# Optimization experiments

Hardware: AMD Instinct MI355X
Metric: run time of the kernel (lower is better)

## Reference

```python
import jax, jax.numpy as jnp
import numpy as np

D_MODEL = 768
D_STATE = 16
D_CONV = 4
EXPAND = 2
D_INNER = EXPAND * D_MODEL
DT_RANK = (D_MODEL + 15) // 16  # 48
BATCH = 2
SEQ = 1024
LN_EPS = 1e-5


def setup_inputs() -> dict:
    key = jax.random.key(0)
    ks = jax.random.split(key, 12)
    s = 0.02
    inp = {
        "x": jax.random.normal(ks[0], (BATCH, SEQ, D_MODEL), dtype=jnp.float32),
        "in_proj_w": jax.random.normal(ks[1], (2 * D_INNER, D_MODEL), dtype=jnp.float32) * s,
        "conv_w": jax.random.normal(ks[2], (D_INNER, D_CONV), dtype=jnp.float32) * s,
        "conv_b": jnp.zeros((D_INNER,), dtype=jnp.float32),
        "x_proj_w": jax.random.normal(ks[3], (DT_RANK + 2 * D_STATE, D_INNER), dtype=jnp.float32) * s,
        "dt_proj_w": jax.random.normal(ks[4], (D_INNER, DT_RANK), dtype=jnp.float32) * s,
        "dt_proj_b": jnp.full((D_INNER,), -4.0, dtype=jnp.float32),  # softplus(-4) ~ small dt
        "A_log": jnp.log(jnp.broadcast_to(jnp.arange(1, D_STATE + 1, dtype=jnp.float32), (D_INNER, D_STATE))),
        "D": jnp.ones((D_INNER,), dtype=jnp.float32),
        "out_proj_w": jax.random.normal(ks[5], (D_MODEL, D_INNER), dtype=jnp.float32) * s,
        "ln_w": jnp.ones((D_MODEL,), dtype=jnp.float32),
        "ln_b": jnp.zeros((D_MODEL,), dtype=jnp.float32),
    }
    return inp


def _mamba(x, in_proj_w, conv_w, conv_b, x_proj_w, dt_proj_w, dt_proj_b, A_log, D, out_proj_w):
    B, L, _ = x.shape
    # input projection -> [B, L, 2*D_INNER], split into x-branch and gate z
    xz = jnp.einsum("bld,ed->ble", x, in_proj_w)
    xb, z = jnp.split(xz, 2, axis=-1)
    # causal depthwise conv1d along L
    lhs = jnp.transpose(xb, (0, 2, 1))  # [B, D_INNER, L]
    rhs = conv_w[:, None, :]  # [D_INNER, 1, D_CONV]
    xc = jax.lax.conv_general_dilated(
        lhs, rhs, window_strides=(1,), padding=[(D_CONV - 1, 0)],
        dimension_numbers=("NCH", "OIH", "NCH"), feature_group_count=D_INNER)
    xc = jnp.transpose(xc, (0, 2, 1)) + conv_b  # [B, L, D_INNER]
    xc = jax.nn.silu(xc)
    # data-dependent SSM parameters
    x_dbl = jnp.einsum("bld,ed->ble", xc, x_proj_w)  # [B, L, DT_RANK+2*D_STATE]
    dt, Bm, Cm = jnp.split(x_dbl, [DT_RANK, DT_RANK + D_STATE], axis=-1)
    dt = jax.nn.softplus(jnp.einsum("blr,dr->bld", dt, dt_proj_w) + dt_proj_b)  # [B, L, D_INNER]
    A = -jnp.exp(A_log)  # [D_INNER, D_STATE]

    # selective scan over time
    def step(h, inp):
        dt_t, B_t, C_t, u_t = inp  # [B,D_INNER], [B,D_STATE], [B,D_STATE], [B,D_INNER]
        dA = jnp.exp(dt_t[:, :, None] * A)  # [B, D_INNER, D_STATE]
        h = h * dA + (dt_t * u_t)[:, :, None] * B_t[:, None, :]
        y = jnp.einsum("bds,bs->bd", h, C_t)
        return h, y

    h0 = jnp.zeros((B, D_INNER, D_STATE), dtype=x.dtype)
    xs = (jnp.transpose(dt, (1, 0, 2)), jnp.transpose(Bm, (1, 0, 2)),
          jnp.transpose(Cm, (1, 0, 2)), jnp.transpose(xc, (1, 0, 2)))
    _, ys = jax.lax.scan(step, h0, xs)  # ys: [L, B, D_INNER]
    y = jnp.transpose(ys, (1, 0, 2)) + xc * D
    y = y * jax.nn.silu(z)
    return jnp.einsum("ble,de->bld", y, out_proj_w)  # [B, L, D_MODEL]


def reference(x, in_proj_w, conv_w, conv_b, x_proj_w, dt_proj_w, dt_proj_b,
              A_log, D, out_proj_w, ln_w, ln_b):
    residual = x
    h = _mamba(x, in_proj_w, conv_w, conv_b, x_proj_w, dt_proj_w, dt_proj_b, A_log, D, out_proj_w)
    # dropout is identity in eval mode
    y = h + residual
    mu = jnp.mean(y, axis=-1, keepdims=True)
    var = jnp.mean(jnp.square(y - mu), axis=-1, keepdims=True)
    return (y - mu) * jax.lax.rsqrt(var + LN_EPS) * ln_w + ln_b
```

## Files before the change

kernel.cpp:

```cpp
#include <hip/hip_runtime.h>
#include <hip/hip_bf16.h>
#include <math.h>

#define BATCH   2
#define SEQ     1024
#define DMODEL  768
#define DINNER  1536
#define DSTATE  16
#define DTRANK  48
#define NTOK    (BATCH*SEQ)
#define XPROJ_N (DTRANK + 2*DSTATE)

#define LC      64
#define NC      (SEQ/LC)

typedef unsigned short ushort_t;
typedef __attribute__((ext_vector_type(8))) short bf16x8;
typedef __attribute__((ext_vector_type(4))) float f32x4;

__device__ __forceinline__ ushort_t f2bf(float f) {
    unsigned int u = __float_as_uint(f);
    u += 0x7FFF + ((u >> 16) & 1);
    return (ushort_t)(u >> 16);
}

__global__ __launch_bounds__(256)
void f2b_3(const float* __restrict__ s0, ushort_t* __restrict__ d0, int n0,
           const float* __restrict__ s1, ushort_t* __restrict__ d1, int n1,
           const float* __restrict__ s2, ushort_t* __restrict__ d2, int n2)
{
    const int i = (blockIdx.x * 256 + threadIdx.x) * 4;
    const float* s; ushort_t* d;
    if (i < n0)               { s = s0 + i;            d = d0 + i; }
    else if (i < n0 + n1)     { s = s1 + (i - n0);     d = d1 + (i - n0); }
    else if (i < n0 + n1 + n2){ s = s2 + (i - n0 - n1);d = d2 + (i - n0 - n1); }
    else return;
    const float4 v = *reinterpret_cast<const float4*>(s);
    ushort4 o;
    o.x = f2bf(v.x); o.y = f2bf(v.y); o.z = f2bf(v.z); o.w = f2bf(v.w);
    *reinterpret_cast<ushort4*>(d) = o;
}

#define GLOAD_LDS16(gp, lp) \
    __builtin_amdgcn_global_load_lds((const __attribute__((address_space(1))) void*)(gp), \
                                     (__attribute__((address_space(3))) void*)(lp), 16, 0, 0)

__global__ __launch_bounds__(256)
void gemm_mfma_bt(const ushort_t* __restrict__ A, const ushort_t* __restrict__ W,
                  float* __restrict__ C, int M, int N, int K)
{
    __shared__ ushort_t As[128 * 32];
    __shared__ ushort_t Bs[128 * 32];

    const int tid  = threadIdx.x;
    const int w    = tid >> 6;
    const int lane = tid & 63;
    const int m0 = blockIdx.y * 128;
    const int n0 = blockIdx.x * 128;

    const int lrow = lane >> 2;
    const int lcol = (lane & 3) * 8;

    const ushort_t* ga0 = A + (size_t)(m0 + w * 16 + lrow) * K + lcol;
    const ushort_t* ga1 = ga0 + (size_t)64 * K;
    const ushort_t* gb0 = W + (size_t)(n0 + w * 16 + lrow) * K + lcol;
    const ushort_t* gb1 = gb0 + (size_t)64 * K;

    ushort_t* lA0 = As + w * 512;
    ushort_t* lA1 = As + 64 * 32 + w * 512;
    ushort_t* lB0 = Bs + w * 512;
    ushort_t* lB1 = Bs + 64 * 32 + w * 512;

    const int wm = w >> 1, wn = w & 1;
    const int fr = lane & 15;
    const int kg = lane >> 4;

    f32x4 acc[4][4] = {};

    for (int kt = 0; kt < K; kt += 32) {
        __syncthreads();
        GLOAD_LDS16(ga0 + kt, lA0);
        GLOAD_LDS16(ga1 + kt, lA1);
        GLOAD_LDS16(gb0 + kt, lB0);
        GLOAD_LDS16(gb1 + kt, lB1);
        __syncthreads();

        bf16x8 af[4], bfr[4];
        #pragma unroll
        for (int i = 0; i < 4; ++i) {
            af[i]  = *reinterpret_cast<const bf16x8*>(&As[(wm * 64 + i * 16 + fr) * 32 + kg * 8]);
            bfr[i] = *reinterpret_cast<const bf16x8*>(&Bs[(wn * 64 + i * 16 + fr) * 32 + kg * 8]);
        }
        #pragma unroll
        for (int i = 0; i < 4; ++i)
            #pragma unroll
            for (int j = 0; j < 4; ++j)
                acc[i][j] = __builtin_amdgcn_mfma_f32_16x16x32_bf16(af[i], bfr[j], acc[i][j], 0, 0, 0);
    }

    #pragma unroll
    for (int i = 0; i < 4; ++i) {
        const int row_base = m0 + wm * 64 + i * 16 + kg * 4;
        #pragma unroll
        for (int j = 0; j < 4; ++j) {
            const int col = n0 + wn * 64 + j * 16 + fr;
            #pragma unroll
            for (int r = 0; r < 4; ++r)
                C[(size_t)(row_base + r) * N + col] = acc[i][j][r];
        }
    }
}

#define BM 64
#define BN 64
#define BK 16

template<int ACT>
__global__ __launch_bounds__(256)
void gemm_tn(const float* __restrict__ A, const float* __restrict__ W,
             const float* __restrict__ bias, float* __restrict__ C,
             int M, int N, int K, int lda)
{
    __shared__ float As[BK][BM + 4];
    __shared__ float Ws[BK][BN + 4];

    const int t  = threadIdx.x;
    const int tx = t & 15;
    const int ty = t >> 4;
    const int row0 = blockIdx.y * BM;
    const int col0 = blockIdx.x * BN;

    const int m_l = t >> 2;
    const int k_l = (t & 3) * 4;

    float acc[4][4] = {};

    for (int kt = 0; kt < K; kt += BK) {
        float4 av, wv;
        {
            const float* ap = A + (size_t)(row0 + m_l) * lda + kt + k_l;
            av = *reinterpret_cast<const float4*>(ap);
        }
        {
            const int wn = col0 + m_l;
            if (wn < N) {
                const float* wp = W + (size_t)wn * K + kt + k_l;
                wv = *reinterpret_cast<const float4*>(wp);
            } else {
                wv = make_float4(0.f, 0.f, 0.f, 0.f);
            }
        }
        __syncthreads();
        As[k_l + 0][m_l] = av.x; As[k_l + 1][m_l] = av.y;
        As[k_l + 2][m_l] = av.z; As[k_l + 3][m_l] = av.w;
        Ws[k_l + 0][m_l] = wv.x; Ws[k_l + 1][m_l] = wv.y;
        Ws[k_l + 2][m_l] = wv.z; Ws[k_l + 3][m_l] = wv.w;
        __syncthreads();

        #pragma unroll
        for (int k = 0; k < BK; ++k) {
            float4 a4 = *reinterpret_cast<const float4*>(&As[k][ty * 4]);
            float4 w4 = *reinterpret_cast<const float4*>(&Ws[k][tx * 4]);
            float af[4] = {a4.x, a4.y, a4.z, a4.w};
            float wf[4] = {w4.x, w4.y, w4.z, w4.w};
            #pragma unroll
            for (int i = 0; i < 4; ++i)
                #pragma unroll
                for (int j = 0; j < 4; ++j)
                    acc[i][j] += af[i] * wf[j];
        }
    }

    #pragma unroll
    for (int i = 0; i < 4; ++i) {
        const int m = row0 + ty * 4 + i;
        #pragma unroll
        for (int j = 0; j < 4; ++j) {
            const int n = col0 + tx * 4 + j;
            if (n < N) {
                float v = acc[i][j];
                if (ACT == 1) {
                    v += bias[n];
                    v = (v > 20.f) ? v : log1pf(expf(v));
                }
                C[(size_t)m * N + n] = v;
            }
        }
    }
}

__global__ __launch_bounds__(256)
void gemm_tn_splitk(const float* __restrict__ A, const float* __restrict__ W,
                    float* __restrict__ C, int M, int N, int K, int lda, int kchunk)
{
    __shared__ float As[BK][BM + 4];
    __shared__ float Ws[BK][BN + 4];

    const int t  = threadIdx.x;
    const int tx = t & 15;
    const int ty = t >> 4;
    const int row0 = blockIdx.y * BM;
    const int col0 = blockIdx.x * BN;
    const int kbeg = blockIdx.z * kchunk;
    const int kend = kbeg + kchunk;

    const int m_l = t >> 2;
    const int k_l = (t & 3) * 4;

    float acc[4][4] = {};

    for (int kt = kbeg; kt < kend; kt += BK) {
        float4 av, wv;
        {
            const float* ap = A + (size_t)(row0 + m_l) * lda + kt + k_l;
            av = *reinterpret_cast<const float4*>(ap);
        }
        {
            const int wn = col0 + m_l;
            if (wn < N) {
                const float* wp = W + (size_t)wn * K + kt + k_l;
                wv = *reinterpret_cast<const float4*>(wp);
            } else {
                wv = make_float4(0.f, 0.f, 0.f, 0.f);
            }
        }
        __syncthreads();
        As[k_l + 0][m_l] = av.x; As[k_l + 1][m_l] = av.y;
        As[k_l + 2][m_l] = av.z; As[k_l + 3][m_l] = av.w;
        Ws[k_l + 0][m_l] = wv.x; Ws[k_l + 1][m_l] = wv.y;
        Ws[k_l + 2][m_l] = wv.z; Ws[k_l + 3][m_l] = wv.w;
        __syncthreads();

        #pragma unroll
        for (int k = 0; k < BK; ++k) {
            float4 a4 = *reinterpret_cast<const float4*>(&As[k][ty * 4]);
            float4 w4 = *reinterpret_cast<const float4*>(&Ws[k][tx * 4]);
            float af[4] = {a4.x, a4.y, a4.z, a4.w};
            float wf[4] = {w4.x, w4.y, w4.z, w4.w};
            #pragma unroll
            for (int i = 0; i < 4; ++i)
                #pragma unroll
                for (int j = 0; j < 4; ++j)
                    acc[i][j] += af[i] * wf[j];
        }
    }

    #pragma unroll
    for (int i = 0; i < 4; ++i) {
        const int m = row0 + ty * 4 + i;
        #pragma unroll
        for (int j = 0; j < 4; ++j) {
            const int n = col0 + tx * 4 + j;
            if (n < N)
                atomicAdd(&C[(size_t)m * N + n], acc[i][j]);
        }
    }
}

__global__ __launch_bounds__(256)
void conv_silu(const float* __restrict__ xz, const float* __restrict__ cw,
               const float* __restrict__ cb, float* __restrict__ xc)
{
    int idx = blockIdx.x * 256 + threadIdx.x;
    if (idx >= NTOK * DINNER) return;
    const int c = idx % DINNER;
    const int m = idx / DINNER;
    const int l = m & (SEQ - 1);

    const float w0 = cw[c * 4 + 0], w1 = cw[c * 4 + 1],
                w2 = cw[c * 4 + 2], w3 = cw[c * 4 + 3];
    const float* base = xz + (size_t)m * (2 * DINNER) + c;

    float acc = cb[c] + base[0] * w3;
    if (l >= 1) acc += base[-(2 * DINNER)]     * w2;
    if (l >= 2) acc += base[-2 * (2 * DINNER)] * w1;
    if (l >= 3) acc += base[-3 * (2 * DINNER)] * w0;

    const float sig = 1.f / (1.f + __expf(-acc));
    xc[idx] = acc * sig;
}

__global__ __launch_bounds__(256)
void scan_chunk_state(const float* __restrict__ dt, const float* __restrict__ xc,
                      const float* __restrict__ xdbl, const float* __restrict__ A_log,
                      float* __restrict__ hA, float* __restrict__ aP)
{
    __shared__ float dt_s[LC * 16];
    __shared__ float xc_s[LC * 16];
    __shared__ float B_s [LC * 16];

    const int c = blockIdx.x;
    const int b = blockIdx.z;
    const int d0 = blockIdx.y * 16;
    const int t  = threadIdx.x;

    const size_t row0 = (size_t)b * SEQ + (size_t)c * LC;

    #pragma unroll
    for (int p = 0; p < (LC * 16) / 256; ++p) {
        const int idx = p * 256 + t;
        const int l = idx >> 4, j = idx & 15;
        const size_t m = row0 + l;
        dt_s[idx] = dt  [m * DINNER  + d0 + j];
        xc_s[idx] = xc  [m * DINNER  + d0 + j];
        B_s [idx] = xdbl[m * XPROJ_N + DTRANK + j];
    }
    __syncthreads();

    const int dl = t >> 4;
    const int s  = t & 15;
    const int d  = d0 + dl;
    const float Aval = -expf(A_log[d * DSTATE + s]);

    float h = 0.f, dts = 0.f;
    #pragma unroll 4
    for (int l = 0; l < LC; ++l) {
        const float dtv = dt_s[l * 16 + dl];
        const float u   = xc_s[l * 16 + dl];
        const float Bv  = B_s [l * 16 + s];
        dts += dtv;
        h = h * __expf(dtv * Aval) + dtv * u * Bv;
    }

    const size_t o = (((size_t)(b * NC + c) * DINNER) + d) * DSTATE + s;
    hA[o] = h;
    aP[o] = __expf(Aval * dts);
}

__global__ __launch_bounds__(256)
void scan_combine(float* __restrict__ hA, const float* __restrict__ aP)
{
    const int idx = blockIdx.x * 256 + threadIdx.x;
    const int b  = idx / (DINNER * DSTATE);
    const int ds = idx % (DINNER * DSTATE);

    float h = 0.f;
    #pragma unroll
    for (int c = 0; c < NC; ++c) {
        const size_t o = ((size_t)(b * NC + c) * DINNER * DSTATE) + ds;
        const float a = hA[o];
        const float p = aP[o];
        hA[o] = h;
        h = a + h * p;
    }
}

__global__ __launch_bounds__(256)
void scan_apply(const float* __restrict__ dt, const float* __restrict__ xc,
                const float* __restrict__ xdbl, const float* __restrict__ xz,
                const float* __restrict__ A_log, const float* __restrict__ Dp,
                const float* __restrict__ hInit, ushort_t* __restrict__ y)
{
    __shared__ float dt_s[LC * 16];
    __shared__ float xc_s[LC * 16];
    __shared__ float B_s [LC * 16];
    __shared__ float C_s [LC * 16];
    __shared__ float z_s [LC * 16];

    const int c = blockIdx.x;
    const int b = blockIdx.z;
    const int d0 = blockIdx.y * 16;
    const int t  = threadIdx.x;

    const size_t row0 = (size_t)b * SEQ + (size_t)c * LC;

    #pragma unroll
    for (int p = 0; p < (LC * 16) / 256; ++p) {
        const int idx = p * 256 + t;
        const int l = idx >> 4, j = idx & 15;
        const size_t m = row0 + l;
        dt_s[idx] = dt  [m * DINNER  + d0 + j];
        xc_s[idx] = xc  [m * DINNER  + d0 + j];
        B_s [idx] = xdbl[m * XPROJ_N + DTRANK + j];
        C_s [idx] = xdbl[m * XPROJ_N + DTRANK + DSTATE + j];
        z_s [idx] = xz  [m * (2 * DINNER) + DINNER + d0 + j];
    }
    __syncthreads();

    const int dl = t >> 4;
    const int s  = t & 15;
    const int d  = d0 + dl;

    const float Aval = -expf(A_log[d * DSTATE + s]);
    const float Dd   = Dp[d];

    const size_t o = (((size_t)(b * NC + c) * DINNER) + d) * DSTATE + s;
    float h = hInit[o];

    #pragma unroll 4
    for (int l = 0; l < LC; ++l) {
        const float dtv = dt_s[l * 16 + dl];
        const float u   = xc_s[l * 16 + dl];
        const float Bv  = B_s [l * 16 + s];
        const float Cv  = C_s [l * 16 + s];

        h = h * __expf(dtv * Aval) + dtv * u * Bv;

        float p = h * Cv;
        p += __shfl_xor(p, 1);
        p += __shfl_xor(p, 2);
        p += __shfl_xor(p, 4);
        p += __shfl_xor(p, 8);

        if (s == 0) {
            const float zv  = z_s[l * 16 + dl];
            const float yv  = p + u * Dd;
            const float sig = 1.f / (1.f + __expf(-zv));
            y[(row0 + l) * DINNER + d] = f2bf(yv * zv * sig);
        }
    }
}

__global__ __launch_bounds__(256)
void ln_kernel(const float* __restrict__ mo, const float* __restrict__ x,
               const float* __restrict__ w, const float* __restrict__ bias,
               float* __restrict__ out)
{
    const int m = blockIdx.x;
    const int t = threadIdx.x;
    const float* mrow = mo + (size_t)m * DMODEL;
    const float* xrow = x  + (size_t)m * DMODEL;

    float v[3];
    float sum = 0.f, ss = 0.f;
    #pragma unroll
    for (int i = 0; i < 3; ++i) {
        const int col = t + 256 * i;
        v[i] = mrow[col] + xrow[col];
        sum += v[i];
        ss  += v[i] * v[i];
    }
    #pragma unroll
    for (int o = 1; o < 64; o <<= 1) {
        sum += __shfl_xor(sum, o);
        ss  += __shfl_xor(ss, o);
    }
    __shared__ float red[2][4];
    const int wid = t >> 6;
    if ((t & 63) == 0) { red[0][wid] = sum; red[1][wid] = ss; }
    __syncthreads();
    sum = red[0][0] + red[0][1] + red[0][2] + red[0][3];
    ss  = red[1][0] + red[1][1] + red[1][2] + red[1][3];

    const float mu   = sum * (1.f / DMODEL);
    const float var  = ss * (1.f / DMODEL) - mu * mu;
    const float rstd = rsqrtf(var + 1e-5f);

    #pragma unroll
    for (int i = 0; i < 3; ++i) {
        const int col = t + 256 * i;
        out[(size_t)m * DMODEL + col] = (v[i] - mu) * rstd * w[col] + bias[col];
    }
}

extern "C" void kernel_launch(void* const* d_in, const int* in_sizes, int n_in,
                              void* d_out, int out_size, void* d_ws, size_t ws_size,
                              hipStream_t stream)
{
    const float* x          = (const float*)d_in[0];
    const float* in_proj_w  = (const float*)d_in[1];
    const float* conv_w     = (const float*)d_in[2];
    const float* conv_b     = (const float*)d_in[3];
    const float* x_proj_w   = (const float*)d_in[4];
    const float* dt_proj_w  = (const float*)d_in[5];
    const float* dt_proj_b  = (const float*)d_in[6];
    const float* A_log      = (const float*)d_in[7];
    const float* Dp         = (const float*)d_in[8];
    const float* out_proj_w = (const float*)d_in[9];
    const float* ln_w       = (const float*)d_in[10];
    const float* ln_b       = (const float*)d_in[11];
    float* out = (float*)d_out;

    float* ws   = (float*)d_ws;
    float* xz   = ws;
    float* xc   = xz   + (size_t)NTOK * 3072;
    float* xdbl = xc   + (size_t)NTOK * 1536;
    float* dt   = xdbl + (size_t)NTOK * 80;
    float* mo   = dt   + (size_t)NTOK * 1536;
    ushort_t* xb16 = (ushort_t*)(mo + (size_t)NTOK * 768);
    ushort_t* ipw16 = xb16  + (size_t)NTOK * DMODEL;
    ushort_t* opw16 = ipw16 + (size_t)2 * DINNER * DMODEL;
    ushort_t* ybb   = opw16 + (size_t)DMODEL * DINNER;

    float* aP = mo;
    float* hA = (float*)d_out;

    {
        const int n0 = NTOK * DMODEL;
        const int n1 = 2 * DINNER * DMODEL;
        const int n2 = DMODEL * DINNER;
        const int nvec = (n0 + n1 + n2) / 4;
        f2b_3<<<(nvec + 255) / 256, 256, 0, stream>>>(
            x, xb16, n0, in_proj_w, ipw16, n1, out_proj_w, opw16, n2);
    }

    gemm_mfma_bt<<<dim3(2 * DINNER / 128, NTOK / 128), 256, 0, stream>>>(
        xb16, ipw16, xz, NTOK, 2 * DINNER, DMODEL);

    conv_silu<<<(NTOK * DINNER) / 256, 256, 0, stream>>>(xz, conv_w, conv_b, xc);

    hipMemsetAsync(xdbl, 0, (size_t)NTOK * XPROJ_N * sizeof(float), stream);
    gemm_tn_splitk<<<dim3((XPROJ_N + BN - 1) / BN, NTOK / BM, 8), 256, 0, stream>>>(
        xc, x_proj_w, xdbl, NTOK, XPROJ_N, DINNER, DINNER, DINNER / 8);

    gemm_tn<1><<<dim3(DINNER / BN, NTOK / BM), 256, 0, stream>>>(
        xdbl, dt_proj_w, dt_proj_b, dt, NTOK, DINNER, DTRANK, XPROJ_N);

    scan_chunk_state<<<dim3(NC, DINNER / 16, BATCH), 256, 0, stream>>>(
        dt, xc, xdbl, A_log, hA, aP);
    scan_combine<<<(BATCH * DINNER * DSTATE) / 256, 256, 0, stream>>>(hA, aP);
    scan_apply<<<dim3(NC, DINNER / 16, BATCH), 256, 0, stream>>>(
        dt, xc, xdbl, xz, A_log, Dp, hA, ybb);

    gemm_mfma_bt<<<dim3(DMODEL / 128, NTOK / 128), 256, 0, stream>>>(
        ybb, opw16, mo, NTOK, DMODEL, DINNER);

    ln_kernel<<<NTOK, 256, 0, stream>>>(mo, x, ln_w, ln_b, out);
}
```

Measured before the change: 293.2 us.

## Restructure chunked scan so each thread owns one channel with all 16 states

The chunk-state and apply scan kernels are remapped so each thread holds all 16 SSM states for one inner channel in registers, instead of one thread per (channel, state) pair. This removes the shuffle-based reduction over states and the shared-memory staging of dt, xc and z, which are now read directly from global memory with coalesced loads. The chunk length is also halved so the grid still has enough blocks. The cost is higher register pressure, longer serial per-thread work, and more chunks for the combine pass.

```diff
diff --git a/kernel.cpp b/kernel.cpp
--- a/kernel.cpp
+++ b/kernel.cpp
@@ -11,7 +11,7 @@
 #define NTOK    (BATCH*SEQ)
 #define XPROJ_N (DTRANK + 2*DSTATE)
 
-#define LC      64
+#define LC      32
 #define NC      (SEQ/LC)
 
 typedef unsigned short ushort_t;
@@ -285,14 +285,13 @@
                       const float* __restrict__ xdbl, const float* __restrict__ A_log,
                       float* __restrict__ hA, float* __restrict__ aP)
 {
-    __shared__ float dt_s[LC * 16];
-    __shared__ float xc_s[LC * 16];
-    __shared__ float B_s [LC * 16];
-
-    const int c = blockIdx.x;
-    const int b = blockIdx.z;
-    const int d0 = blockIdx.y * 16;
+    __shared__ float B_s[LC * 16];
+
+    const int c  = blockIdx.x;
+    const int d0 = blockIdx.y * 256;
+    const int b  = blockIdx.z;
     const int t  = threadIdx.x;
+    const int d  = d0 + t;
 
     const size_t row0 = (size_t)b * SEQ + (size_t)c * LC;
 
@@ -300,31 +299,50 @@
     for (int p = 0; p < (LC * 16) / 256; ++p) {
         const int idx = p * 256 + t;
         const int l = idx >> 4, j = idx & 15;
+        B_s[idx] = xdbl[(row0 + l) * XPROJ_N + DTRANK + j];
+    }
+    __syncthreads();
+
+    float Aval[16];
+    #pragma unroll
+    for (int q = 0; q < 4; ++q) {
+        const float4 a4 = *reinterpret_cast<const float4*>(&A_log[(size_t)d * DSTATE + q * 4]);
+        Aval[q*4+0] = -expf(a4.x); Aval[q*4+1] = -expf(a4.y);
+        Aval[q*4+2] = -expf(a4.z); Aval[q*4+3] = -expf(a4.w);
+    }
+
+    float h[16];
+    #pragma unroll
+    for (int s = 0; s < 16; ++s) h[s] = 0.f;
+    float dts = 0.f;
+
+    #pragma unroll 2
+    for (int l = 0; l < LC; ++l) {
         const size_t m = row0 + l;
-        dt_s[idx] = dt  [m * DINNER  + d0 + j];
-        xc_s[idx] = xc  [m * DINNER  + d0 + j];
-        B_s [idx] = xdbl[m * XPROJ_N + DTRANK + j];
-    }
-    __syncthreads();
-
-    const int dl = t >> 4;
-    const int s  = t & 15;
-    const int d  = d0 + dl;
-    const float Aval = -expf(A_log[d * DSTATE + s]);
-
-    float h = 0.f, dts = 0.f;
-    #pragma unroll 4
-    for (int l = 0; l < LC; ++l) {
-        const float dtv = dt_s[l * 16 + dl];
-        const float u   = xc_s[l * 16 + dl];
-        const float Bv  = B_s [l * 16 + s];
+        const float dtv = dt[m * DINNER + d];
+        const float u   = xc[m * DINNER + d];
+        const float du  = dtv * u;
         dts += dtv;
-        h = h * __expf(dtv * Aval) + dtv * u * Bv;
-    }
-
-    const size_t o = (((size_t)(b * NC + c) * DINNER) + d) * DSTATE + s;
-    hA[o] = h;
-    aP[o] = __expf(Aval * dts);
+        float Bv[16];
+        #pragma unroll
+        for (int q = 0; q < 4; ++q) {
+            const float4 b4 = *reinterpret_cast<const float4*>(&B_s[l * 16 + q * 4]);
+            Bv[q*4+0] = b4.x; Bv[q*4+1] = b4.y; Bv[q*4+2] = b4.z; Bv[q*4+3] = b4.w;
+        }
+        #pragma unroll
+        for (int s = 0; s < 16; ++s)
+            h[s] = h[s] * __expf(dtv * Aval[s]) + du * Bv[s];
+    }
+
+    const size_t o = (((size_t)(b * NC + c) * DINNER) + d) * DSTATE;
+    #pragma unroll
+    for (int q = 0; q < 4; ++q) {
+        float4 hv = make_float4(h[q*4+0], h[q*4+1], h[q*4+2], h[q*4+3]);
+        float4 pv = make_float4(__expf(Aval[q*4+0]*dts), __expf(Aval[q*4+1]*dts),
+                                __expf(Aval[q*4+2]*dts), __expf(Aval[q*4+3]*dts));
+        *reinterpret_cast<float4*>(&hA[o + q*4]) = hv;
+        *reinterpret_cast<float4*>(&aP[o + q*4]) = pv;
+    }
 }
 
 __global__ __launch_bounds__(256)
@@ -351,16 +369,14 @@
                 const float* __restrict__ A_log, const float* __restrict__ Dp,
                 const float* __restrict__ hInit, ushort_t* __restrict__ y)
 {
-    __shared__ float dt_s[LC * 16];
-    __shared__ float xc_s[LC * 16];
-    __shared__ float B_s [LC * 16];
-    __shared__ float C_s [LC * 16];
-    __shared__ float z_s [LC * 16];
-
-    const int c = blockIdx.x;
-    const int b = blockIdx.z;
-    const int d0 = blockIdx.y * 16;
+    __shared__ float B_s[LC * 16];
+    __shared__ float C_s[LC * 16];
+
+    const int c  = blockIdx.x;
+    const int d0 = blockIdx.y * 256;
+    const int b  = blockIdx.z;
     const int t  = threadIdx.x;
+    const int d  = d0 + t;
 
     const size_t row0 = (size_t)b * SEQ + (size_t)c * LC;
 
@@ -368,46 +384,54 @@
     for (int p = 0; p < (LC * 16) / 256; ++p) {
         const int idx = p * 256 + t;
         const int l = idx >> 4, j = idx & 15;
+        B_s[idx] = xdbl[(row0 + l) * XPROJ_N + DTRANK + j];
+        C_s[idx] = xdbl[(row0 + l) * XPROJ_N + DTRANK + DSTATE + j];
+    }
+    __syncthreads();
+
+    float Aval[16];
+    #pragma unroll
+    for (int q = 0; q < 4; ++q) {
+        const float4 a4 = *reinterpret_cast<const float4*>(&A_log[(size_t)d * DSTATE + q * 4]);
+        Aval[q*4+0] = -expf(a4.x); Aval[q*4+1] = -expf(a4.y);
+        Aval[q*4+2] = -expf(a4.z); Aval[q*4+3] = -expf(a4.w);
+    }
+    const float Dd = Dp[d];
+
+    const size_t o = (((size_t)(b * NC + c) * DINNER) + d) * DSTATE;
+    float h[16];
+    #pragma unroll
+    for (int q = 0; q < 4; ++q) {
+        const float4 h4 = *reinterpret_cast<const float4*>(&hInit[o + q*4]);
+        h[q*4+0] = h4.x; h[q*4+1] = h4.y; h[q*4+2] = h4.z; h[q*4+3] = h4.w;
+    }
+
+    #pragma unroll 2
+    for (int l = 0; l < LC; ++l) {
         const size_t m = row0 + l;
-        dt_s[idx] = dt  [m * DINNER  + d0 + j];
-        xc_s[idx] = xc  [m * DINNER  + d0 + j];
-        B_s [idx] = xdbl[m * XPROJ_N + DTRANK + j];
-        C_s [idx] = xdbl[m * XPROJ_N + DTRANK + DSTATE + j];
-        z_s [idx] = xz  [m * (2 * DINNER) + DINNER + d0 + j];
-    }
-    __syncthreads();
-
-    const int dl = t >> 4;
-    const int s  = t & 15;
-    const int d  = d0 + dl;
-
-    const float Aval = -expf(A_log[d * DSTATE + s]);
-    const float Dd   = Dp[d];
-
-    const size_t o = (((size_t)(b * NC + c) * DINNER) + d) * DSTATE + s;
-    float h = hInit[o];
-
-    #pragma unroll 4
-    for (int l = 0; l < LC; ++l) {
-        const float dtv = dt_s[l * 16 + dl];
-        const float u   = xc_s[l * 16 + dl];
-        const float Bv  = B_s [l * 16 + s];
-        const float Cv  = C_s [l * 16 + s];
-
-        h = h * __expf(dtv * Aval) + dtv * u * Bv;
-
-        float p = h * Cv;
-        p += __shfl_xor(p, 1);
-        p += __shfl_xor(p, 2);
-        p += __shfl_xor(p, 4);
-        p += __shfl_xor(p, 8);
-
-        if (s == 0) {
-            const float zv  = z_s[l * 16 + dl];
-            const float yv  = p + u * Dd;
-            const float sig = 1.f / (1.f + __expf(-zv));
-            y[(row0 + l) * DINNER + d] = f2bf(yv * zv * sig);
-        }
+        const float dtv = dt[m * DINNER + d];
+        const float u   = xc[m * DINNER + d];
+        const float zv  = xz[m * (2 * DINNER) + DINNER + d];
+        const float du  = dtv * u;
+
+        float acc = 0.f;
+        #pragma unroll
+        for (int q = 0; q < 4; ++q) {
+            const float4 b4 = *reinterpret_cast<const float4*>(&B_s[l * 16 + q * 4]);
+            const float4 c4 = *reinterpret_cast<const float4*>(&C_s[l * 16 + q * 4]);
+            const float bb[4] = {b4.x, b4.y, b4.z, b4.w};
+            const float cc[4] = {c4.x, c4.y, c4.z, c4.w};
+            #pragma unroll
+            for (int r = 0; r < 4; ++r) {
+                const int s = q * 4 + r;
+                h[s] = h[s] * __expf(dtv * Aval[s]) + du * bb[r];
+                acc += h[s] * cc[r];
+            }
+        }
+
+        const float yv  = acc + u * Dd;
+        const float sig = 1.f / (1.f + __expf(-zv));
+        y[m * DINNER + d] = f2bf(yv * zv * sig);
     }
 }
 
@@ -506,10 +530,10 @@
     gemm_tn<1><<<dim3(DINNER / BN, NTOK / BM), 256, 0, stream>>>(
         xdbl, dt_proj_w, dt_proj_b, dt, NTOK, DINNER, DTRANK, XPROJ_N);
 
-    scan_chunk_state<<<dim3(NC, DINNER / 16, BATCH), 256, 0, stream>>>(
+    scan_chunk_state<<<dim3(NC, DINNER / 256, BATCH), 256, 0, stream>>>(
         dt, xc, xdbl, A_log, hA, aP);
     scan_combine<<<(BATCH * DINNER * DSTATE) / 256, 256, 0, stream>>>(hA, aP);
-    scan_apply<<<dim3(NC, DINNER / 16, BATCH), 256, 0, stream>>>(
+    scan_apply<<<dim3(NC, DINNER / 256, BATCH), 256, 0, stream>>>(
         dt, xc, xdbl, xz, A_log, Dp, hA, ybb);
 
     gemm_mfma_bt<<<dim3(DMODEL / 128, NTOK / 128), 256, 0, stream>>>(
```

New measurement: 274.6 us. 6.3% less time.
